# Performance work log

Hardware: AMD Instinct MI355X
Metric: run time of the kernel (lower is better)

The kernel has to match this reference:

```python
import jax, jax.numpy as jnp
import numpy as np

N = 10000
E = 640000
C = 128   # in_channels
H = 512   # hidden_dim
O = 128   # out_channels


def setup_inputs() -> dict:
    key = jax.random.key(0)
    k1, k2, k3, k4, k5, k6, k7 = jax.random.split(key, 7)
    x = jax.random.normal(k1, (N, C), dtype=jnp.float32)
    edge_index = jax.random.randint(k2, (2, E), 0, N, dtype=jnp.int64)
    # MLP params (Linear(2C, H) -> ReLU -> Linear(H, O)), torch default init scale
    w1 = jax.random.uniform(k3, (2 * C, H), jnp.float32, -1, 1) / np.sqrt(2 * C)
    b1 = jax.random.uniform(k4, (H,), jnp.float32, -1, 1) / np.sqrt(2 * C)
    w2 = jax.random.uniform(k5, (H, O), jnp.float32, -1, 1) / np.sqrt(H)
    b2 = jax.random.uniform(k6, (O,), jnp.float32, -1, 1) / np.sqrt(H)
    return {"x": x, "edge_index": edge_index, "w1": w1, "b1": b1, "w2": w2, "b2": b2}


def reference(x, edge_index, w1, b1, w2, b2):
    row, col = edge_index[0], edge_index[1]
    # scatter_mean: mean of source features x[col] into destination row
    summed = jax.ops.segment_sum(x[col], row, num_segments=N)          # [N, C]
    count = jax.ops.segment_sum(jnp.ones((E,), x.dtype), row, num_segments=N)
    neighbor_mean = summed / jnp.maximum(count, 1.0)[:, None]          # [N, C]
    h = jnp.concatenate([x, neighbor_mean], axis=1)                    # [N, 2C]
    h = jax.nn.relu(h @ w1 + b1)                                       # [N, H]
    return h @ w2 + b2                                                 # [N, O]
```

## Files before the change

### kernel.cpp

```cpp
#include <hip/hip_runtime.h>

#define C_IN 128
#define H_DIM 512
#define O_DIM 128
#define CAP   128
#define PAD   16
#define BM    32

typedef __attribute__((ext_vector_type(8))) short short8;
typedef __attribute__((ext_vector_type(4))) float f32x4;

__device__ inline unsigned short f2bf(float f) {
    unsigned int u = __float_as_uint(f);
    unsigned int r = (u + 0x7FFF + ((u >> 16) & 1)) >> 16;
    return (unsigned short)r;
}
__device__ inline float bf2f(unsigned short s) {
    return __uint_as_float(((unsigned int)s) << 16);
}

__device__ inline void tr_tile(const float* __restrict__ src, unsigned short* __restrict__ dst,
                               int R, int Ccols, int bx, int by) {
    __shared__ float tile[32][33];
    const int c0 = bx * 32, r0 = by * 32;
    const int tx = threadIdx.x & 31, ty = threadIdx.x >> 5;
#pragma unroll
    for (int i = 0; i < 32; i += 8)
        tile[ty + i][tx] = src[(long)(r0 + ty + i) * Ccols + c0 + tx];
    __syncthreads();
#pragma unroll
    for (int i = 0; i < 32; i += 8)
        dst[(long)(c0 + ty + i) * R + r0 + tx] = f2bf(tile[tx][ty + i]);
}

__global__ __launch_bounds__(256)
void prep_fill(const float* __restrict__ w1, unsigned short* __restrict__ w1t,
               const float* __restrict__ w2, unsigned short* __restrict__ w2t,
               const float* __restrict__ x, unsigned short* __restrict__ h0,
               const int* __restrict__ ei, int* __restrict__ cnt_p,
               unsigned short* __restrict__ bucket, int N, int E) {
    const int bid = blockIdx.x;
    if (bid < 192) {
        if (bid < 128) tr_tile(w1, w1t, 2 * C_IN, H_DIM, bid & 15, bid >> 4);
        else { int j = bid - 128; tr_tile(w2, w2t, H_DIM, O_DIM, j & 3, j >> 2); }
    }

    const int XJ = N * C_IN / 4;
    const int FJ = (E + 3) / 4;
    const int gtid = bid * 256 + threadIdx.x;
    const int nthr = gridDim.x * 256;
    const bool al = ((E & 3) == 0);
    for (int j = gtid; j < XJ + FJ; j += nthr) {
        if (j < XJ) {
            int n = j >> 5, c4 = j & 31;
            float4 v = ((const float4*)x)[j];
            ushort4 s;
            s.x = f2bf(v.x); s.y = f2bf(v.y); s.z = f2bf(v.z); s.w = f2bf(v.w);
            *(ushort4*)(h0 + (long)n * (2 * C_IN) + c4 * 4) = s;
        } else {
            int e = (j - XJ) * 4;
            if (al) {
                int4 r = *(const int4*)(ei + e);
                int4 c = *(const int4*)(ei + E + e);
                int s0 = atomicAdd(&cnt_p[r.x * PAD], 1);
                int s1 = atomicAdd(&cnt_p[r.y * PAD], 1);
                int s2 = atomicAdd(&cnt_p[r.z * PAD], 1);
                int s3 = atomicAdd(&cnt_p[r.w * PAD], 1);
                if (s0 < CAP) bucket[(long)r.x * CAP + s0] = (unsigned short)c.x;
                if (s1 < CAP) bucket[(long)r.y * CAP + s1] = (unsigned short)c.y;
                if (s2 < CAP) bucket[(long)r.z * CAP + s2] = (unsigned short)c.z;
                if (s3 < CAP) bucket[(long)r.w * CAP + s3] = (unsigned short)c.w;
            } else {
                for (int k = e; k < E && k < e + 4; k++) {
                    int row = ei[k];
                    int col = ei[E + k];
                    int slot = atomicAdd(&cnt_p[row * PAD], 1);
                    if (slot < CAP) bucket[(long)row * CAP + slot] = (unsigned short)col;
                }
            }
        }
    }
}

__global__ __launch_bounds__(256)
void gather_kernel(const unsigned short* __restrict__ bucket,
                   const int* __restrict__ cnt_p, unsigned short* __restrict__ h0,
                   int N) {
    const int lane = threadIdx.x & 63;
    const int n = blockIdx.x * 4 + (threadIdx.x >> 6);
    if (n >= N) return;
    const int g = lane >> 4;
    const int l16 = lane & 15;
    const int degt = cnt_p[n * PAD];
    const int deg = min(degt, CAP);

    const unsigned int bb = ((const unsigned int*)bucket)[(long)n * (CAP / 2) + lane];

    float acc[8] = {};
    int e = 0;
    for (; e + 32 <= deg; e += 32) {
        int c[8];
#pragma unroll
        for (int i = 0; i < 8; i++) {
            int k = e + 4 * i + g;
            c[i] = (__shfl(bb, k >> 1) >> ((k & 1) << 4)) & 0xffff;
        }
        short8 u[8];
#pragma unroll
        for (int i = 0; i < 8; i++)
            u[i] = *(const short8*)(h0 + (long)c[i] * (2 * C_IN) + l16 * 8);
#pragma unroll
        for (int j = 0; j < 8; j++) {
            float s0 = bf2f((unsigned short)u[0][j]) + bf2f((unsigned short)u[1][j]);
            float s1 = bf2f((unsigned short)u[2][j]) + bf2f((unsigned short)u[3][j]);
            float s2 = bf2f((unsigned short)u[4][j]) + bf2f((unsigned short)u[5][j]);
            float s3 = bf2f((unsigned short)u[6][j]) + bf2f((unsigned short)u[7][j]);
            acc[j] += (s0 + s1) + (s2 + s3);
        }
    }
    if (e + 16 <= deg) {
        int k0 = e + g, k1 = e + 4 + g, k2 = e + 8 + g, k3 = e + 12 + g;
        int c0 = (__shfl(bb, k0 >> 1) >> ((k0 & 1) << 4)) & 0xffff;
        int c1 = (__shfl(bb, k1 >> 1) >> ((k1 & 1) << 4)) & 0xffff;
        int c2 = (__shfl(bb, k2 >> 1) >> ((k2 & 1) << 4)) & 0xffff;
        int c3 = (__shfl(bb, k3 >> 1) >> ((k3 & 1) << 4)) & 0xffff;
        short8 u0 = *(const short8*)(h0 + (long)c0 * (2 * C_IN) + l16 * 8);
        short8 u1 = *(const short8*)(h0 + (long)c1 * (2 * C_IN) + l16 * 8);
        short8 u2 = *(const short8*)(h0 + (long)c2 * (2 * C_IN) + l16 * 8);
        short8 u3 = *(const short8*)(h0 + (long)c3 * (2 * C_IN) + l16 * 8);
#pragma unroll
        for (int j = 0; j < 8; j++)
            acc[j] += (bf2f((unsigned short)u0[j]) + bf2f((unsigned short)u1[j]))
                    + (bf2f((unsigned short)u2[j]) + bf2f((unsigned short)u3[j]));
        e += 16;
    }
    if (e + 8 <= deg) {
        int k0 = e + g, k1 = e + 4 + g;
        int c0 = (__shfl(bb, k0 >> 1) >> ((k0 & 1) << 4)) & 0xffff;
        int c1 = (__shfl(bb, k1 >> 1) >> ((k1 & 1) << 4)) & 0xffff;
        short8 u0 = *(const short8*)(h0 + (long)c0 * (2 * C_IN) + l16 * 8);
        short8 u1 = *(const short8*)(h0 + (long)c1 * (2 * C_IN) + l16 * 8);
#pragma unroll
        for (int j = 0; j < 8; j++)
            acc[j] += bf2f((unsigned short)u0[j]) + bf2f((unsigned short)u1[j]);
        e += 8;
    }
    if (e + 4 <= deg) {
        int k = e + g;
        int c = (__shfl(bb, k >> 1) >> ((k & 1) << 4)) & 0xffff;
        short8 u = *(const short8*)(h0 + (long)c * (2 * C_IN) + l16 * 8);
#pragma unroll
        for (int j = 0; j < 8; j++) acc[j] += bf2f((unsigned short)u[j]);
        e += 4;
    }
    {
        int rem = deg - e;
        int k = e + g;
        unsigned int bv = __shfl(bb, k >> 1);
        if (g < rem) {
            int c = (bv >> ((k & 1) << 4)) & 0xffff;
            short8 u = *(const short8*)(h0 + (long)c * (2 * C_IN) + l16 * 8);
#pragma unroll
            for (int j = 0; j < 8; j++) acc[j] += bf2f((unsigned short)u[j]);
        }
    }
#pragma unroll
    for (int j = 0; j < 8; j++) {
        acc[j] += __shfl_xor(acc[j], 16, 64);
        acc[j] += __shfl_xor(acc[j], 32, 64);
    }
    if (lane < 16) {
        float inv = 1.0f / fmaxf((float)degt, 1.0f);
        short8 mv;
#pragma unroll
        for (int j = 0; j < 8; j++) mv[j] = (short)f2bf(acc[j] * inv);
        *(short8*)(h0 + (long)n * (2 * C_IN) + C_IN + l16 * 8) = mv;
    }
}

__global__ __launch_bounds__(256)
void fused_mlp(const unsigned short* __restrict__ h0,
               const unsigned short* __restrict__ w1t,
               const float* __restrict__ bias1,
               const unsigned short* __restrict__ w2t,
               const float* __restrict__ bias2,
               float* __restrict__ out, int M) {
    __shared__ __align__(16) unsigned short h1s[BM][520];

    const int t = threadIdx.x;
    const int m0 = blockIdx.x * BM;
    const int lane = t & 63;
    const int w = t >> 6;
    const int l16 = lane & 15;
    const int q = lane >> 4;
    const int q8 = q * 8;

    short8 a_reg[2][8];
#pragma unroll
    for (int mf = 0; mf < 2; mf++) {
        int gm = m0 + mf * 16 + l16;
        if (gm < M) {
            const unsigned short* ap = h0 + (long)gm * (2 * C_IN) + q8;
#pragma unroll
            for (int s = 0; s < 8; s++) a_reg[mf][s] = *(const short8*)(ap + s * 32);
        } else {
#pragma unroll
            for (int s = 0; s < 8; s++) a_reg[mf][s] = short8{};
        }
    }

#pragma unroll
    for (int nc = 0; nc < 4; nc++) {
        const int colbase = w * 128 + nc * 32;
        f32x4 acc[2][2] = {};
#pragma unroll
        for (int s = 0; s < 8; s++) {
            short8 b0 = *(const short8*)(w1t + (long)(colbase + l16) * 256 + s * 32 + q8);
            short8 b1 = *(const short8*)(w1t + (long)(colbase + 16 + l16) * 256 + s * 32 + q8);
            acc[0][0] = __builtin_amdgcn_mfma_f32_16x16x32_bf16(a_reg[0][s], b0, acc[0][0], 0, 0, 0);
            acc[0][1] = __builtin_amdgcn_mfma_f32_16x16x32_bf16(a_reg[0][s], b1, acc[0][1], 0, 0, 0);
            acc[1][0] = __builtin_amdgcn_mfma_f32_16x16x32_bf16(a_reg[1][s], b0, acc[1][0], 0, 0, 0);
            acc[1][1] = __builtin_amdgcn_mfma_f32_16x16x32_bf16(a_reg[1][s], b1, acc[1][1], 0, 0, 0);
        }
        float bb0 = bias1[colbase + l16];
        float bb1 = bias1[colbase + 16 + l16];
#pragma unroll
        for (int mf = 0; mf < 2; mf++) {
#pragma unroll
            for (int r = 0; r < 4; r++) {
                int m = mf * 16 + q * 4 + r;
                h1s[m][colbase + l16]      = f2bf(fmaxf(acc[mf][0][r] + bb0, 0.f));
                h1s[m][colbase + 16 + l16] = f2bf(fmaxf(acc[mf][1][r] + bb1, 0.f));
            }
        }
    }
    __syncthreads();

    f32x4 acc2[2][2] = {};
    const int wn = w * 32;
#pragma unroll
    for (int ks = 0; ks < 16; ks++) {
        short8 a0 = *(const short8*)&h1s[l16][ks * 32 + q8];
        short8 a1 = *(const short8*)&h1s[16 + l16][ks * 32 + q8];
        short8 b0 = *(const short8*)(w2t + (long)(wn + l16) * H_DIM + ks * 32 + q8);
        short8 b1 = *(const short8*)(w2t + (long)(wn + 16 + l16) * H_DIM + ks * 32 + q8);
        acc2[0][0] = __builtin_amdgcn_mfma_f32_16x16x32_bf16(a0, b0, acc2[0][0], 0, 0, 0);
        acc2[0][1] = __builtin_amdgcn_mfma_f32_16x16x32_bf16(a0, b1, acc2[0][1], 0, 0, 0);
        acc2[1][0] = __builtin_amdgcn_mfma_f32_16x16x32_bf16(a1, b0, acc2[1][0], 0, 0, 0);
        acc2[1][1] = __builtin_amdgcn_mfma_f32_16x16x32_bf16(a1, b1, acc2[1][1], 0, 0, 0);
    }
#pragma unroll
    for (int mf = 0; mf < 2; mf++) {
#pragma unroll
        for (int nf = 0; nf < 2; nf++) {
            int gn = wn + nf * 16 + l16;
            float bb = bias2[gn];
#pragma unroll
            for (int r = 0; r < 4; r++) {
                int gm = m0 + mf * 16 + q * 4 + r;
                if (gm < M) out[(long)gm * O_DIM + gn] = acc2[mf][nf][r] + bb;
            }
        }
    }
}

extern "C" void kernel_launch(void* const* d_in, const int* in_sizes, int n_in,
                              void* d_out, int out_size, void* d_ws, size_t ws_size,
                              hipStream_t stream) {
    const float* x  = (const float*)d_in[0];
    const int*   ei = (const int*)d_in[1];
    const float* w1 = (const float*)d_in[2];
    const float* b1 = (const float*)d_in[3];
    const float* w2 = (const float*)d_in[4];
    const float* b2 = (const float*)d_in[5];
    float* out = (float*)d_out;

    const int N = in_sizes[0] / C_IN;
    const int E = in_sizes[1] / 2;

    unsigned short* h0b = (unsigned short*)d_ws;
    unsigned short* w1t = h0b + (size_t)N * (2 * C_IN);
    unsigned short* w2t = w1t + (size_t)H_DIM * (2 * C_IN);
    int* cnt_p = (int*)(w2t + (size_t)O_DIM * H_DIM);
    unsigned short* bucket = (unsigned short*)(cnt_p + (size_t)N * PAD);

    hipMemsetAsync(cnt_p, 0, (size_t)N * PAD * sizeof(int), stream);
    prep_fill<<<1024, 256, 0, stream>>>(w1, w1t, w2, w2t, x, h0b, ei, cnt_p, bucket, N, E);
    gather_kernel<<<(N + 3) / 4, 256, 0, stream>>>(bucket, cnt_p, h0b, N);
    fused_mlp<<<(N + BM - 1) / BM, 256, 0, stream>>>(h0b, w1t, b1, w2t, b2, out, N);
}
```

Baseline: 139.1 us.

## Bucket edges with per-block LDS histograms and bulk global slot reservation

Edge bucketing moves to 16 dedicated 1024-thread blocks. Each block builds a per-row shared-memory histogram of its edge slice, reserves slot ranges in the global counters with one atomic per non-empty row, then places column indices using LDS atomics. The padded counter array shrinks to one dense int per row, and the remaining blocks do the weight transposes and the x-to-bf16 conversion. This cuts contended global atomics, but the edge work now runs on only 16 workgroups and reads edge_index twice, which may limit parallelism.

```diff
diff --git a/kernel.cpp b/kernel.cpp
--- a/kernel.cpp
+++ b/kernel.cpp
@@ -4,8 +4,10 @@
 #define H_DIM 512
 #define O_DIM 128
 #define CAP   128
-#define PAD   16
 #define BM    32
+#define FB    16
+#define FBT   1024
+#define HCAP  10240
 
 typedef __attribute__((ext_vector_type(8))) short short8;
 typedef __attribute__((ext_vector_type(4))) float f32x4;
@@ -19,79 +21,84 @@
     return __uint_as_float(((unsigned int)s) << 16);
 }
 
-__device__ inline void tr_tile(const float* __restrict__ src, unsigned short* __restrict__ dst,
-                               int R, int Ccols, int bx, int by) {
-    __shared__ float tile[32][33];
-    const int c0 = bx * 32, r0 = by * 32;
-    const int tx = threadIdx.x & 31, ty = threadIdx.x >> 5;
-#pragma unroll
-    for (int i = 0; i < 32; i += 8)
-        tile[ty + i][tx] = src[(long)(r0 + ty + i) * Ccols + c0 + tx];
-    __syncthreads();
-#pragma unroll
-    for (int i = 0; i < 32; i += 8)
-        dst[(long)(c0 + ty + i) * R + r0 + tx] = f2bf(tile[tx][ty + i]);
-}
-
-__global__ __launch_bounds__(256)
+union SMem {
+    float tile[32][33];
+    int   hist[HCAP];
+};
+
+__global__ __launch_bounds__(FBT)
 void prep_fill(const float* __restrict__ w1, unsigned short* __restrict__ w1t,
                const float* __restrict__ w2, unsigned short* __restrict__ w2t,
                const float* __restrict__ x, unsigned short* __restrict__ h0,
-               const int* __restrict__ ei, int* __restrict__ cnt_p,
+               const int* __restrict__ ei, int* __restrict__ cnt,
                unsigned short* __restrict__ bucket, int N, int E) {
+    __shared__ SMem sm;
     const int bid = blockIdx.x;
-    if (bid < 192) {
-        if (bid < 128) tr_tile(w1, w1t, 2 * C_IN, H_DIM, bid & 15, bid >> 4);
-        else { int j = bid - 128; tr_tile(w2, w2t, H_DIM, O_DIM, j & 3, j >> 2); }
-    }
-
-    const int XJ = N * C_IN / 4;
-    const int FJ = (E + 3) / 4;
-    const int gtid = bid * 256 + threadIdx.x;
-    const int nthr = gridDim.x * 256;
-    const bool al = ((E & 3) == 0);
-    for (int j = gtid; j < XJ + FJ; j += nthr) {
-        if (j < XJ) {
+    const int t = threadIdx.x;
+
+    if (bid < FB) {
+        const int epb = (E + FB - 1) / FB;
+        const int e0 = bid * epb;
+        const int e1 = min(E, e0 + epb);
+        if (N <= HCAP) {
+            for (int r = t; r < N; r += FBT) sm.hist[r] = 0;
+            __syncthreads();
+            for (int k = e0 + t; k < e1; k += FBT)
+                atomicAdd(&sm.hist[ei[k]], 1);
+            __syncthreads();
+            for (int r = t; r < N; r += FBT) {
+                int c = sm.hist[r];
+                if (c > 0) sm.hist[r] = atomicAdd(&cnt[r], c);
+            }
+            __syncthreads();
+            for (int k = e0 + t; k < e1; k += FBT) {
+                int row = ei[k];
+                int col = ei[E + k];
+                int slot = atomicAdd(&sm.hist[row], 1);
+                if (slot < CAP) bucket[(long)row * CAP + slot] = (unsigned short)col;
+            }
+        } else {
+            for (int k = e0 + t; k < e1; k += FBT) {
+                int row = ei[k];
+                int col = ei[E + k];
+                int slot = atomicAdd(&cnt[row], 1);
+                if (slot < CAP) bucket[(long)row * CAP + slot] = (unsigned short)col;
+            }
+        }
+    } else {
+        const int pb = bid - FB;
+        if (pb < 192) {
+            const int tx = t & 31, ty = t >> 5;
+            const float* src; unsigned short* dst; int R, Ccols, bx, by;
+            if (pb < 128) { src = w1; dst = w1t; R = 2 * C_IN; Ccols = H_DIM; bx = pb & 15; by = pb >> 4; }
+            else { int j = pb - 128; src = w2; dst = w2t; R = H_DIM; Ccols = O_DIM; bx = j & 3; by = j >> 2; }
+            const int c0 = bx * 32, r0 = by * 32;
+            sm.tile[ty][tx] = src[(long)(r0 + ty) * Ccols + c0 + tx];
+            __syncthreads();
+            dst[(long)(c0 + ty) * R + r0 + tx] = f2bf(sm.tile[tx][ty]);
+        }
+        const int nb = gridDim.x - FB;
+        const int XJ = N * C_IN / 4;
+        for (int j = pb * FBT + t; j < XJ; j += nb * FBT) {
             int n = j >> 5, c4 = j & 31;
             float4 v = ((const float4*)x)[j];
             ushort4 s;
             s.x = f2bf(v.x); s.y = f2bf(v.y); s.z = f2bf(v.z); s.w = f2bf(v.w);
             *(ushort4*)(h0 + (long)n * (2 * C_IN) + c4 * 4) = s;
-        } else {
-            int e = (j - XJ) * 4;
-            if (al) {
-                int4 r = *(const int4*)(ei + e);
-                int4 c = *(const int4*)(ei + E + e);
-                int s0 = atomicAdd(&cnt_p[r.x * PAD], 1);
-                int s1 = atomicAdd(&cnt_p[r.y * PAD], 1);
-                int s2 = atomicAdd(&cnt_p[r.z * PAD], 1);
-                int s3 = atomicAdd(&cnt_p[r.w * PAD], 1);
-                if (s0 < CAP) bucket[(long)r.x * CAP + s0] = (unsigned short)c.x;
-                if (s1 < CAP) bucket[(long)r.y * CAP + s1] = (unsigned short)c.y;
-                if (s2 < CAP) bucket[(long)r.z * CAP + s2] = (unsigned short)c.z;
-                if (s3 < CAP) bucket[(long)r.w * CAP + s3] = (unsigned short)c.w;
-            } else {
-                for (int k = e; k < E && k < e + 4; k++) {
-                    int row = ei[k];
-                    int col = ei[E + k];
-                    int slot = atomicAdd(&cnt_p[row * PAD], 1);
-                    if (slot < CAP) bucket[(long)row * CAP + slot] = (unsigned short)col;
-                }
-            }
         }
     }
 }
 
 __global__ __launch_bounds__(256)
 void gather_kernel(const unsigned short* __restrict__ bucket,
-                   const int* __restrict__ cnt_p, unsigned short* __restrict__ h0,
+                   const int* __restrict__ cnt, unsigned short* __restrict__ h0,
                    int N) {
     const int lane = threadIdx.x & 63;
     const int n = blockIdx.x * 4 + (threadIdx.x >> 6);
     if (n >= N) return;
     const int g = lane >> 4;
     const int l16 = lane & 15;
-    const int degt = cnt_p[n * PAD];
+    const int degt = cnt[n];
     const int deg = min(degt, CAP);
 
     const unsigned int bb = ((const unsigned int*)bucket)[(long)n * (CAP / 2) + lane];
@@ -281,11 +288,11 @@
     unsigned short* h0b = (unsigned short*)d_ws;
     unsigned short* w1t = h0b + (size_t)N * (2 * C_IN);
     unsigned short* w2t = w1t + (size_t)H_DIM * (2 * C_IN);
-    int* cnt_p = (int*)(w2t + (size_t)O_DIM * H_DIM);
-    unsigned short* bucket = (unsigned short*)(cnt_p + (size_t)N * PAD);
-
-    hipMemsetAsync(cnt_p, 0, (size_t)N * PAD * sizeof(int), stream);
-    prep_fill<<<1024, 256, 0, stream>>>(w1, w1t, w2, w2t, x, h0b, ei, cnt_p, bucket, N, E);
-    gather_kernel<<<(N + 3) / 4, 256, 0, stream>>>(bucket, cnt_p, h0b, N);
+    int* cnt = (int*)(w2t + (size_t)O_DIM * H_DIM);
+    unsigned short* bucket = (unsigned short*)(cnt + (size_t)N);
+
+    hipMemsetAsync(cnt, 0, (size_t)N * sizeof(int), stream);
+    prep_fill<<<FB + 240, FBT, 0, stream>>>(w1, w1t, w2, w2t, x, h0b, ei, cnt, bucket, N, E);
+    gather_kernel<<<(N + 3) / 4, 256, 0, stream>>>(bucket, cnt, h0b, N);
     fused_mlp<<<(N + BM - 1) / BM, 256, 0, stream>>>(h0b, w1t, b1, w2t, b2, out, N);
 }
```

Result: slower. 166.2 us (+19.5%).

## Fuse neighbor-mean gather into MLP kernel and drop padded counters

Applied to the files above, without the earlier changes.

Merges the gather kernel into the MLP kernel. Each 512-thread block computes neighbor means for its 32 rows into shared memory and then runs both GEMMs, so the mean half of h0 is never written to or read back from global memory and one launch is removed. The per-node counters are no longer padded to 16 ints, which shrinks the memset but puts several counters on the same cache line under atomics. The edge-fill work is also moved ahead of the x conversion in the grid-stride loop. The MLP work is split across 8 waves instead of 4, and gather parallelism per block is now tied to the MLP tiling, with only 313 blocks.

```diff
diff --git a/kernel.cpp b/kernel.cpp
--- a/kernel.cpp
+++ b/kernel.cpp
@@ -4,7 +4,6 @@
 #define H_DIM 512
 #define O_DIM 128
 #define CAP   128
-#define PAD   16
 #define BM    32
 
 typedef __attribute__((ext_vector_type(8))) short short8;
@@ -36,8 +35,8 @@
 __global__ __launch_bounds__(256)
 void prep_fill(const float* __restrict__ w1, unsigned short* __restrict__ w1t,
                const float* __restrict__ w2, unsigned short* __restrict__ w2t,
-               const float* __restrict__ x, unsigned short* __restrict__ h0,
-               const int* __restrict__ ei, int* __restrict__ cnt_p,
+               const float* __restrict__ x, unsigned short* __restrict__ xb,
+               const int* __restrict__ ei, int* __restrict__ cnt,
                unsigned short* __restrict__ bucket, int N, int E) {
     const int bid = blockIdx.x;
     if (bid < 192) {
@@ -45,27 +44,21 @@
         else { int j = bid - 128; tr_tile(w2, w2t, H_DIM, O_DIM, j & 3, j >> 2); }
     }
 
+    const int FJ = (E + 3) / 4;
     const int XJ = N * C_IN / 4;
-    const int FJ = (E + 3) / 4;
     const int gtid = bid * 256 + threadIdx.x;
     const int nthr = gridDim.x * 256;
     const bool al = ((E & 3) == 0);
-    for (int j = gtid; j < XJ + FJ; j += nthr) {
-        if (j < XJ) {
-            int n = j >> 5, c4 = j & 31;
-            float4 v = ((const float4*)x)[j];
-            ushort4 s;
-            s.x = f2bf(v.x); s.y = f2bf(v.y); s.z = f2bf(v.z); s.w = f2bf(v.w);
-            *(ushort4*)(h0 + (long)n * (2 * C_IN) + c4 * 4) = s;
-        } else {
-            int e = (j - XJ) * 4;
+    for (int j = gtid; j < FJ + XJ; j += nthr) {
+        if (j < FJ) {
+            int e = j * 4;
             if (al) {
                 int4 r = *(const int4*)(ei + e);
                 int4 c = *(const int4*)(ei + E + e);
-                int s0 = atomicAdd(&cnt_p[r.x * PAD], 1);
-                int s1 = atomicAdd(&cnt_p[r.y * PAD], 1);
-                int s2 = atomicAdd(&cnt_p[r.z * PAD], 1);
-                int s3 = atomicAdd(&cnt_p[r.w * PAD], 1);
+                int s0 = atomicAdd(&cnt[r.x], 1);
+                int s1 = atomicAdd(&cnt[r.y], 1);
+                int s2 = atomicAdd(&cnt[r.z], 1);
+                int s3 = atomicAdd(&cnt[r.w], 1);
                 if (s0 < CAP) bucket[(long)r.x * CAP + s0] = (unsigned short)c.x;
                 if (s1 < CAP) bucket[(long)r.y * CAP + s1] = (unsigned short)c.y;
                 if (s2 < CAP) bucket[(long)r.z * CAP + s2] = (unsigned short)c.z;
@@ -74,144 +67,160 @@
                 for (int k = e; k < E && k < e + 4; k++) {
                     int row = ei[k];
                     int col = ei[E + k];
-                    int slot = atomicAdd(&cnt_p[row * PAD], 1);
+                    int slot = atomicAdd(&cnt[row], 1);
                     if (slot < CAP) bucket[(long)row * CAP + slot] = (unsigned short)col;
                 }
             }
-        }
-    }
-}
-
-__global__ __launch_bounds__(256)
-void gather_kernel(const unsigned short* __restrict__ bucket,
-                   const int* __restrict__ cnt_p, unsigned short* __restrict__ h0,
-                   int N) {
-    const int lane = threadIdx.x & 63;
-    const int n = blockIdx.x * 4 + (threadIdx.x >> 6);
-    if (n >= N) return;
-    const int g = lane >> 4;
-    const int l16 = lane & 15;
-    const int degt = cnt_p[n * PAD];
-    const int deg = min(degt, CAP);
-
-    const unsigned int bb = ((const unsigned int*)bucket)[(long)n * (CAP / 2) + lane];
-
-    float acc[8] = {};
-    int e = 0;
-    for (; e + 32 <= deg; e += 32) {
-        int c[8];
-#pragma unroll
-        for (int i = 0; i < 8; i++) {
-            int k = e + 4 * i + g;
-            c[i] = (__shfl(bb, k >> 1) >> ((k & 1) << 4)) & 0xffff;
-        }
-        short8 u[8];
-#pragma unroll
-        for (int i = 0; i < 8; i++)
-            u[i] = *(const short8*)(h0 + (long)c[i] * (2 * C_IN) + l16 * 8);
-#pragma unroll
-        for (int j = 0; j < 8; j++) {
-            float s0 = bf2f((unsigned short)u[0][j]) + bf2f((unsigned short)u[1][j]);
-            float s1 = bf2f((unsigned short)u[2][j]) + bf2f((unsigned short)u[3][j]);
-            float s2 = bf2f((unsigned short)u[4][j]) + bf2f((unsigned short)u[5][j]);
-            float s3 = bf2f((unsigned short)u[6][j]) + bf2f((unsigned short)u[7][j]);
-            acc[j] += (s0 + s1) + (s2 + s3);
-        }
-    }
-    if (e + 16 <= deg) {
-        int k0 = e + g, k1 = e + 4 + g, k2 = e + 8 + g, k3 = e + 12 + g;
-        int c0 = (__shfl(bb, k0 >> 1) >> ((k0 & 1) << 4)) & 0xffff;
-        int c1 = (__shfl(bb, k1 >> 1) >> ((k1 & 1) << 4)) & 0xffff;
-        int c2 = (__shfl(bb, k2 >> 1) >> ((k2 & 1) << 4)) & 0xffff;
-        int c3 = (__shfl(bb, k3 >> 1) >> ((k3 & 1) << 4)) & 0xffff;
-        short8 u0 = *(const short8*)(h0 + (long)c0 * (2 * C_IN) + l16 * 8);
-        short8 u1 = *(const short8*)(h0 + (long)c1 * (2 * C_IN) + l16 * 8);
-        short8 u2 = *(const short8*)(h0 + (long)c2 * (2 * C_IN) + l16 * 8);
-        short8 u3 = *(const short8*)(h0 + (long)c3 * (2 * C_IN) + l16 * 8);
-#pragma unroll
-        for (int j = 0; j < 8; j++)
-            acc[j] += (bf2f((unsigned short)u0[j]) + bf2f((unsigned short)u1[j]))
-                    + (bf2f((unsigned short)u2[j]) + bf2f((unsigned short)u3[j]));
-        e += 16;
-    }
-    if (e + 8 <= deg) {
-        int k0 = e + g, k1 = e + 4 + g;
-        int c0 = (__shfl(bb, k0 >> 1) >> ((k0 & 1) << 4)) & 0xffff;
-        int c1 = (__shfl(bb, k1 >> 1) >> ((k1 & 1) << 4)) & 0xffff;
-        short8 u0 = *(const short8*)(h0 + (long)c0 * (2 * C_IN) + l16 * 8);
-        short8 u1 = *(const short8*)(h0 + (long)c1 * (2 * C_IN) + l16 * 8);
-#pragma unroll
-        for (int j = 0; j < 8; j++)
-            acc[j] += bf2f((unsigned short)u0[j]) + bf2f((unsigned short)u1[j]);
-        e += 8;
-    }
-    if (e + 4 <= deg) {
-        int k = e + g;
-        int c = (__shfl(bb, k >> 1) >> ((k & 1) << 4)) & 0xffff;
-        short8 u = *(const short8*)(h0 + (long)c * (2 * C_IN) + l16 * 8);
-#pragma unroll
-        for (int j = 0; j < 8; j++) acc[j] += bf2f((unsigned short)u[j]);
-        e += 4;
-    }
-    {
-        int rem = deg - e;
-        int k = e + g;
-        unsigned int bv = __shfl(bb, k >> 1);
-        if (g < rem) {
-            int c = (bv >> ((k & 1) << 4)) & 0xffff;
-            short8 u = *(const short8*)(h0 + (long)c * (2 * C_IN) + l16 * 8);
-#pragma unroll
-            for (int j = 0; j < 8; j++) acc[j] += bf2f((unsigned short)u[j]);
-        }
-    }
-#pragma unroll
-    for (int j = 0; j < 8; j++) {
-        acc[j] += __shfl_xor(acc[j], 16, 64);
-        acc[j] += __shfl_xor(acc[j], 32, 64);
-    }
-    if (lane < 16) {
-        float inv = 1.0f / fmaxf((float)degt, 1.0f);
-        short8 mv;
-#pragma unroll
-        for (int j = 0; j < 8; j++) mv[j] = (short)f2bf(acc[j] * inv);
-        *(short8*)(h0 + (long)n * (2 * C_IN) + C_IN + l16 * 8) = mv;
-    }
-}
-
-__global__ __launch_bounds__(256)
-void fused_mlp(const unsigned short* __restrict__ h0,
-               const unsigned short* __restrict__ w1t,
-               const float* __restrict__ bias1,
-               const unsigned short* __restrict__ w2t,
-               const float* __restrict__ bias2,
-               float* __restrict__ out, int M) {
+        } else {
+            int jc = j - FJ;
+            int n = jc >> 5, c4 = jc & 31;
+            float4 v = ((const float4*)x)[jc];
+            ushort4 s;
+            s.x = f2bf(v.x); s.y = f2bf(v.y); s.z = f2bf(v.z); s.w = f2bf(v.w);
+            *(ushort4*)(xb + (long)n * C_IN + c4 * 4) = s;
+        }
+    }
+}
+
+__global__ __launch_bounds__(512)
+void gather_mlp(const unsigned short* __restrict__ xb,
+                const unsigned short* __restrict__ bucket,
+                const int* __restrict__ cnt,
+                const unsigned short* __restrict__ w1t,
+                const float* __restrict__ bias1,
+                const unsigned short* __restrict__ w2t,
+                const float* __restrict__ bias2,
+                float* __restrict__ out, int N) {
     __shared__ __align__(16) unsigned short h1s[BM][520];
+    __shared__ __align__(16) unsigned short mean_s[BM][136];
 
     const int t = threadIdx.x;
     const int m0 = blockIdx.x * BM;
     const int lane = t & 63;
-    const int w = t >> 6;
+    const int wv = t >> 6;
     const int l16 = lane & 15;
     const int q = lane >> 4;
     const int q8 = q * 8;
 
+    for (int i = 0; i < 4; i++) {
+        const int n = m0 + wv * 4 + i;
+        if (n >= N) break;
+        const int degt = cnt[n];
+        const int deg = min(degt, CAP);
+        const unsigned int bb = ((const unsigned int*)bucket)[(long)n * (CAP / 2) + lane];
+
+        float acc[8] = {};
+        int e = 0;
+        for (; e + 32 <= deg; e += 32) {
+            int c[8];
+#pragma unroll
+            for (int ii = 0; ii < 8; ii++) {
+                int k = e + 4 * ii + q;
+                c[ii] = (__shfl(bb, k >> 1) >> ((k & 1) << 4)) & 0xffff;
+            }
+            short8 u[8];
+#pragma unroll
+            for (int ii = 0; ii < 8; ii++)
+                u[ii] = *(const short8*)(xb + (long)c[ii] * C_IN + l16 * 8);
+#pragma unroll
+            for (int j = 0; j < 8; j++) {
+                float s0 = bf2f((unsigned short)u[0][j]) + bf2f((unsigned short)u[1][j]);
+                float s1 = bf2f((unsigned short)u[2][j]) + bf2f((unsigned short)u[3][j]);
+                float s2 = bf2f((unsigned short)u[4][j]) + bf2f((unsigned short)u[5][j]);
+                float s3 = bf2f((unsigned short)u[6][j]) + bf2f((unsigned short)u[7][j]);
+                acc[j] += (s0 + s1) + (s2 + s3);
+            }
+        }
+        if (e + 16 <= deg) {
+            int k0 = e + q, k1 = e + 4 + q, k2 = e + 8 + q, k3 = e + 12 + q;
+            int c0 = (__shfl(bb, k0 >> 1) >> ((k0 & 1) << 4)) & 0xffff;
+            int c1 = (__shfl(bb, k1 >> 1) >> ((k1 & 1) << 4)) & 0xffff;
+            int c2 = (__shfl(bb, k2 >> 1) >> ((k2 & 1) << 4)) & 0xffff;
+            int c3 = (__shfl(bb, k3 >> 1) >> ((k3 & 1) << 4)) & 0xffff;
+            short8 u0 = *(const short8*)(xb + (long)c0 * C_IN + l16 * 8);
+            short8 u1 = *(const short8*)(xb + (long)c1 * C_IN + l16 * 8);
+            short8 u2 = *(const short8*)(xb + (long)c2 * C_IN + l16 * 8);
+            short8 u3 = *(const short8*)(xb + (long)c3 * C_IN + l16 * 8);
+#pragma unroll
+            for (int j = 0; j < 8; j++)
+                acc[j] += (bf2f((unsigned short)u0[j]) + bf2f((unsigned short)u1[j]))
+                        + (bf2f((unsigned short)u2[j]) + bf2f((unsigned short)u3[j]));
+            e += 16;
+        }
+        if (e + 8 <= deg) {
+            int k0 = e + q, k1 = e + 4 + q;
+            int c0 = (__shfl(bb, k0 >> 1) >> ((k0 & 1) << 4)) & 0xffff;
+            int c1 = (__shfl(bb, k1 >> 1) >> ((k1 & 1) << 4)) & 0xffff;
+            short8 u0 = *(const short8*)(xb + (long)c0 * C_IN + l16 * 8);
+            short8 u1 = *(const short8*)(xb + (long)c1 * C_IN + l16 * 8);
+#pragma unroll
+            for (int j = 0; j < 8; j++)
+                acc[j] += bf2f((unsigned short)u0[j]) + bf2f((unsigned short)u1[j]);
+            e += 8;
+        }
+        if (e + 4 <= deg) {
+            int k = e + q;
+            int c = (__shfl(bb, k >> 1) >> ((k & 1) << 4)) & 0xffff;
+            short8 u = *(const short8*)(xb + (long)c * C_IN + l16 * 8);
+#pragma unroll
+            for (int j = 0; j < 8; j++) acc[j] += bf2f((unsigned short)u[j]);
+            e += 4;
+        }
+        {
+            int rem = deg - e;
+            int k = e + q;
+            unsigned int bv = __shfl(bb, k >> 1);
+            if (q < rem) {
+                int c = (bv >> ((k & 1) << 4)) & 0xffff;
+                short8 u = *(const short8*)(xb + (long)c * C_IN + l16 * 8);
+#pragma unroll
+                for (int j = 0; j < 8; j++) acc[j] += bf2f((unsigned short)u[j]);
+            }
+        }
+#pragma unroll
+        for (int j = 0; j < 8; j++) {
+            acc[j] += __shfl_xor(acc[j], 16, 64);
+            acc[j] += __shfl_xor(acc[j], 32, 64);
+        }
+        if (lane < 16) {
+            float inv = 1.0f / fmaxf((float)degt, 1.0f);
+            short8 mv;
+#pragma unroll
+            for (int j = 0; j < 8; j++) mv[j] = (short)f2bf(acc[j] * inv);
+            *(short8*)&mean_s[n - m0][l16 * 8] = mv;
+        }
+    }
+
     short8 a_reg[2][8];
 #pragma unroll
     for (int mf = 0; mf < 2; mf++) {
         int gm = m0 + mf * 16 + l16;
-        if (gm < M) {
-            const unsigned short* ap = h0 + (long)gm * (2 * C_IN) + q8;
-#pragma unroll
-            for (int s = 0; s < 8; s++) a_reg[mf][s] = *(const short8*)(ap + s * 32);
+        if (gm < N) {
+            const unsigned short* ap = xb + (long)gm * C_IN + q8;
+#pragma unroll
+            for (int s = 0; s < 4; s++) a_reg[mf][s] = *(const short8*)(ap + s * 32);
         } else {
 #pragma unroll
-            for (int s = 0; s < 8; s++) a_reg[mf][s] = short8{};
-        }
-    }
-
-#pragma unroll
-    for (int nc = 0; nc < 4; nc++) {
-        const int colbase = w * 128 + nc * 32;
+            for (int s = 0; s < 4; s++) a_reg[mf][s] = short8{};
+        }
+    }
+    __syncthreads();
+#pragma unroll
+    for (int mf = 0; mf < 2; mf++) {
+        int gm = m0 + mf * 16 + l16;
+        if (gm < N) {
+#pragma unroll
+            for (int s = 4; s < 8; s++)
+                a_reg[mf][s] = *(const short8*)&mean_s[mf * 16 + l16][(s - 4) * 32 + q8];
+        } else {
+#pragma unroll
+            for (int s = 4; s < 8; s++) a_reg[mf][s] = short8{};
+        }
+    }
+
+#pragma unroll
+    for (int nc = 0; nc < 2; nc++) {
+        const int colbase = wv * 64 + nc * 32;
         f32x4 acc[2][2] = {};
 #pragma unroll
         for (int s = 0; s < 8; s++) {
@@ -236,30 +245,24 @@
     }
     __syncthreads();
 
-    f32x4 acc2[2][2] = {};
-    const int wn = w * 32;
+    f32x4 acc2[2] = {};
+    const int wn = wv * 16;
 #pragma unroll
     for (int ks = 0; ks < 16; ks++) {
         short8 a0 = *(const short8*)&h1s[l16][ks * 32 + q8];
         short8 a1 = *(const short8*)&h1s[16 + l16][ks * 32 + q8];
         short8 b0 = *(const short8*)(w2t + (long)(wn + l16) * H_DIM + ks * 32 + q8);
-        short8 b1 = *(const short8*)(w2t + (long)(wn + 16 + l16) * H_DIM + ks * 32 + q8);
-        acc2[0][0] = __builtin_amdgcn_mfma_f32_16x16x32_bf16(a0, b0, acc2[0][0], 0, 0, 0);
-        acc2[0][1] = __builtin_amdgcn_mfma_f32_16x16x32_bf16(a0, b1, acc2[0][1], 0, 0, 0);
-        acc2[1][0] = __builtin_amdgcn_mfma_f32_16x16x32_bf16(a1, b0, acc2[1][0], 0, 0, 0);
-        acc2[1][1] = __builtin_amdgcn_mfma_f32_16x16x32_bf16(a1, b1, acc2[1][1], 0, 0, 0);
-    }
+        acc2[0] = __builtin_amdgcn_mfma_f32_16x16x32_bf16(a0, b0, acc2[0], 0, 0, 0);
+        acc2[1] = __builtin_amdgcn_mfma_f32_16x16x32_bf16(a1, b0, acc2[1], 0, 0, 0);
+    }
+    const int gn = wn + l16;
+    const float bb = bias2[gn];
 #pragma unroll
     for (int mf = 0; mf < 2; mf++) {
 #pragma unroll
-        for (int nf = 0; nf < 2; nf++) {
-            int gn = wn + nf * 16 + l16;
-            float bb = bias2[gn];
-#pragma unroll
-            for (int r = 0; r < 4; r++) {
-                int gm = m0 + mf * 16 + q * 4 + r;
-                if (gm < M) out[(long)gm * O_DIM + gn] = acc2[mf][nf][r] + bb;
-            }
+        for (int r = 0; r < 4; r++) {
+            int gm = m0 + mf * 16 + q * 4 + r;
+            if (gm < N) out[(long)gm * O_DIM + gn] = acc2[mf][r] + bb;
         }
     }
 }
@@ -278,14 +281,13 @@
     const int N = in_sizes[0] / C_IN;
     const int E = in_sizes[1] / 2;
 
-    unsigned short* h0b = (unsigned short*)d_ws;
-    unsigned short* w1t = h0b + (size_t)N * (2 * C_IN);
+    unsigned short* xb = (unsigned short*)d_ws;
+    unsigned short* w1t = xb + (size_t)N * C_IN;
     unsigned short* w2t = w1t + (size_t)H_DIM * (2 * C_IN);
-    int* cnt_p = (int*)(w2t + (size_t)O_DIM * H_DIM);
-    unsigned short* bucket = (unsigned short*)(cnt_p + (size_t)N * PAD);
-
-    hipMemsetAsync(cnt_p, 0, (size_t)N * PAD * sizeof(int), stream);
-    prep_fill<<<1024, 256, 0, stream>>>(w1, w1t, w2, w2t, x, h0b, ei, cnt_p, bucket, N, E);
-    gather_kernel<<<(N + 3) / 4, 256, 0, stream>>>(bucket, cnt_p, h0b, N);
-    fused_mlp<<<(N + BM - 1) / BM, 256, 0, stream>>>(h0b, w1t, b1, w2t, b2, out, N);
-}
+    int* cnt = (int*)(w2t + (size_t)O_DIM * H_DIM);
+    unsigned short* bucket = (unsigned short*)(cnt + (size_t)N);
+
+    hipMemsetAsync(cnt, 0, (size_t)N * sizeof(int), stream);
+    prep_fill<<<1024, 256, 0, stream>>>(w1, w1t, w2, w2t, x, xb, ei, cnt, bucket, N, E);
+    gather_mlp<<<(N + BM - 1) / BM, 512, 0, stream>>>(xb, bucket, cnt, w1t, b1, w2t, b2, out, N);
+}
```

Result: slower. 151.9 us (+9.2%).
